# Optimization experiments

Hardware: AMD Instinct MI355X
Metric: run time of the kernel (lower is better)

The kernel has to match this reference:

```python
import jax, jax.numpy as jnp
import numpy as np

KH = KW = 3
STRIDE = 1
PAD = 1
DIL = 1


def _bilinear_sample(img, py, px):
    Hin, Win = img.shape[-2], img.shape[-1]
    y0 = jnp.floor(py)
    x0 = jnp.floor(px)
    y0i = y0.astype(jnp.int32)
    x0i = x0.astype(jnp.int32)
    wy = py - y0
    wx = px - x0

    def get(yi, xi):
        valid = (yi >= 0) & (yi < Hin) & (xi >= 0) & (xi < Win)
        yc = jnp.clip(yi, 0, Hin - 1)
        xc = jnp.clip(xi, 0, Win - 1)
        v = img[:, yc, xc]  # [C, K, H, W]
        return v * valid[None].astype(img.dtype)

    v00 = get(y0i, x0i)
    v01 = get(y0i, x0i + 1)
    v10 = get(y0i + 1, x0i)
    v11 = get(y0i + 1, x0i + 1)
    return (v00 * (1 - wy) * (1 - wx) + v01 * (1 - wy) * wx
            + v10 * wy * (1 - wx) + v11 * wy * wx)  # [C, K, H, W]


def _deform_conv(input, offset, mask, weight, bias):
    B, C, H, W = input.shape
    outH = (H + 2 * PAD - DIL * (KH - 1) - 1) // STRIDE + 1
    outW = (W + 2 * PAD - DIL * (KW - 1) - 1) // STRIDE + 1
    K = KH * KW
    # NOTE: DepthOffset in the original source overwrites its computed
    # depth-guided offsets with zeros and detaches them, so the effective
    # sampling offset is just `offset` (standard modulated deform conv, DCNv2).
    off = offset.reshape(B, K, 2, outH, outW)
    off_y = off[:, :, 0]  # [B, K, outH, outW]
    off_x = off[:, :, 1]
    ky = (jnp.arange(K) // KW) * DIL  # kernel-tap row offsets
    kx = (jnp.arange(K) % KW) * DIL
    ys = jnp.arange(outH) * STRIDE - PAD
    xs = jnp.arange(outW) * STRIDE - PAD
    base_y = (ky[:, None, None] + ys[None, :, None]).astype(input.dtype)  # [K, outH, 1]
    base_x = (kx[:, None, None] + xs[None, None, :]).astype(input.dtype)  # [K, 1, outW]
    py = base_y[None] + off_y  # [B, K, outH, outW]
    px = base_x[None] + off_x
    cols = jax.vmap(_bilinear_sample)(input, py, px)  # [B, C, K, outH, outW]
    cols = cols * mask[:, None]  # modulate by mask [B, 1, K, outH, outW]
    out = jnp.einsum('bckhw,ock->bohw', cols, weight.reshape(weight.shape[0], C, K))
    return out + bias[None, :, None, None]


def setup_inputs() -> dict:
    key = jax.random.key(0)
    ks = jax.random.split(key, 6)
    B, C, H, W = 4, 64, 128, 128
    O = 64
    fan_in = C * KH * KW
    bound = 1.0 / np.sqrt(fan_in)
    return {
        'input': jax.random.normal(ks[0], (B, C, H, W), dtype=jnp.float32),
        'depth': jax.random.uniform(ks[1], (B, 1, H, W), dtype=jnp.float32),
        'offset': jax.random.normal(ks[2], (B, 18, H, W), dtype=jnp.float32),
        'mask': jax.random.uniform(ks[3], (B, 9, H, W), dtype=jnp.float32),
        'weight': jax.random.uniform(ks[4], (O, C, KH, KW), dtype=jnp.float32,
                                     minval=-bound, maxval=bound),
        'bias': jax.random.uniform(ks[5], (O,), dtype=jnp.float32,
                                   minval=-bound, maxval=bound),
    }


def reference(input, depth, offset, mask, weight, bias):
    # depth-guided offsets are computed then zeroed+detached in the original
    # module, so depth does not influence the output.
    return _deform_conv(input, offset, mask, weight, bias)
```

## Files before the change

### kernel.cpp

```cpp
#include <hip/hip_runtime.h>


typedef __attribute__((ext_vector_type(8))) short bf16x8;
typedef __attribute__((ext_vector_type(4))) float f32x4;
typedef __attribute__((ext_vector_type(2))) float f32x2;
typedef __attribute__((ext_vector_type(4))) unsigned int u32x4;

#define HH 128
#define WW 128
#define CC 64
#define OO 64
#define HW (128 * 128)

__device__ __forceinline__ unsigned f32_to_bf16_rne(float f) {
    unsigned u = __float_as_uint(f);
    return (u + 0x7FFFu + ((u >> 16) & 1u)) >> 16;
}

__device__ __forceinline__ unsigned cvtpk_bf16(float lo, float hi) {
    unsigned r;
    asm("v_cvt_pk_bf16_f32 %0, %1, %2" : "=v"(r) : "v"(lo), "v"(hi));
    return r;
}

__global__ __launch_bounds__(256)
void prep_fused18(const float* __restrict__ input,
                  unsigned short* __restrict__ nhwc,
                  const float* __restrict__ weight,
                  unsigned short* __restrict__ wT2)
{
    __shared__ unsigned tile[64][33];
    const int tid = threadIdx.x;
    const int blk = blockIdx.x;

    if (blk >= 2048) {
        const int d  = (blk - 2048) * 256 + tid;
        const int o  = d & 63;
        const int k8 = d >> 6;
        const int kt = k8 >> 3;
        const int c8 = k8 & 7;
        u32x4 pk;
        #pragma unroll
        for (int jj = 0; jj < 4; ++jj) {
            unsigned lo = f32_to_bf16_rne(weight[o * 576 + (c8 * 8 + 2 * jj)     * 9 + kt]);
            unsigned hi = f32_to_bf16_rne(weight[o * 576 + (c8 * 8 + 2 * jj + 1) * 9 + kt]);
            pk[jj] = lo | (hi << 16);
        }
        *(u32x4*)(wT2 + (size_t)d * 8) = pk;
        return;
    }

    const int b  = blk >> 9;
    const int y  = (blk >> 2) & 127;
    const int xbase = (blk & 3) * 32;
    #pragma unroll
    for (int it = 0; it < 2; ++it) {
        int flat = it * 256 + tid;
        int c = flat >> 3, x4 = flat & 7;
        const f32x4 v = *(const f32x4*)(input + ((b * 64 + c) * 128 + y) * 128 + xbase + x4 * 4);
        tile[c][x4 * 4 + 0] = f32_to_bf16_rne(v[0]);
        tile[c][x4 * 4 + 1] = f32_to_bf16_rne(v[1]);
        tile[c][x4 * 4 + 2] = f32_to_bf16_rne(v[2]);
        tile[c][x4 * 4 + 3] = f32_to_bf16_rne(v[3]);
    }
    __syncthreads();
    {
        int x = tid >> 3, cg = tid & 7;
        unsigned r0 = tile[cg * 8 + 0][x], r1 = tile[cg * 8 + 1][x];
        unsigned r2 = tile[cg * 8 + 2][x], r3 = tile[cg * 8 + 3][x];
        unsigned r4 = tile[cg * 8 + 4][x], r5 = tile[cg * 8 + 5][x];
        unsigned r6 = tile[cg * 8 + 6][x], r7 = tile[cg * 8 + 7][x];
        u32x4 pk;
        pk[0] = r0 | (r1 << 16); pk[1] = r2 | (r3 << 16);
        pk[2] = r4 | (r5 << 16); pk[3] = r6 | (r7 << 16);
        *(u32x4*)(nhwc + ((size_t)((b * 128 + y) * 128 + xbase + x)) * 64 + cg * 8) = pk;
    }
}

__global__ __launch_bounds__(1024)
void ddc_order18(const unsigned short* __restrict__ nhwc,
                 const unsigned short* __restrict__ wT2,
                 const float* __restrict__ offset,
                 const float* __restrict__ mask,
                 const float* __restrict__ bias,
                 float* __restrict__ out)
{
    __shared__ u32x4 win[8192];
    __shared__ float sten[6912];

    const int blk0 = blockIdx.x;
    const int blk  = (blk0 & 7) * 32 + (blk0 >> 3);
    const int b    = blk >> 6;
    const int h0   = (blk & 63) * 2;
    const int ys   = h0 - 3;
    const int tid  = threadIdx.x;
    const int wave = tid >> 6;
    const int lane = tid & 63;
    const int l15  = lane & 15;
    const int kq   = lane >> 4;
    const int hr   = wave >> 3;
    const int h    = h0 + hr;
    const int wpix = (wave & 7) * 16 + l15;

    f32x4 acc[4];
    #pragma unroll
    for (int mt = 0; mt < 4; ++mt) acc[mt] = (f32x4){0.f, 0.f, 0.f, 0.f};

    const unsigned short* nb = nhwc + (size_t)b * HW * CC;
    const u32x4* wsrc = (const u32x4*)wT2;

    #pragma unroll
    for (int it = 0; it < 7; ++it) {
        const int f = it * 1024 + tid;
        if (f < 6912) {
            const int plane = f >> 8;
            const int fr    = (f >> 7) & 1;
            const int x     = f & 127;
            sten[f] = (plane < 18)
                ? offset[((b * 18 + plane)      * 128 + (h0 + fr)) * 128 + x]
                : mask  [((b * 9 + (plane - 18))* 128 + (h0 + fr)) * 128 + x];
        }
    }

    #pragma unroll
    for (int slot = 0; slot < 8; ++slot) {
        const int y = ys + slot;
        if (y >= 0 && y < HH) {
            const int q  = tid;
            const int x  = q >> 3;
            const int c8 = q & 7;
            win[slot * 1024 + q] =
                *(const u32x4*)(nb + ((size_t)(y * WW + x)) * CC + ((c8 ^ (x & 7)) << 3));
        }
    }
    __syncthreads();

    #pragma unroll
    for (int kt = 0; kt < 9; ++kt) {
        const u32x4* wpa = wsrc + (kt * 8 + kq)     * 64 + l15;
        const u32x4* wpb = wsrc + (kt * 8 + 4 + kq) * 64 + l15;
        const u32x4 wa0 = wpa[0], wa1 = wpa[16], wa2 = wpa[32], wa3 = wpa[48];
        const u32x4 wb0 = wpb[0], wb1 = wpb[16], wb2 = wpb[32], wb3 = wpb[48];

        const float oy = sten[(2 * kt)     * 256 + hr * 128 + wpix];
        const float ox = sten[(2 * kt + 1) * 256 + hr * 128 + wpix];
        const float m  = sten[(18 + kt)    * 256 + hr * 128 + wpix];

        const float py = (float)(h - 1 + kt / 3) + oy;
        const float px = (float)(wpix - 1 + kt % 3) + ox;
        const float y0f = floorf(py), x0f = floorf(px);
        const int y0 = (int)y0f, x0 = (int)x0f;
        const float wy = py - y0f, wx = px - x0f;
        const int y1 = y0 + 1, x1 = x0 + 1;
        const bool vy0 = (y0 >= 0) & (y0 < HH);
        const bool vy1 = (y1 >= 0) & (y1 < HH);
        const bool vx0 = (x0 >= 0) & (x0 < WW);
        const bool vx1 = (x1 >= 0) & (x1 < WW);
        const int y0c = min(max(y0, 0), HH - 1), y1c = min(max(y1, 0), HH - 1);
        const int x0c = min(max(x0, 0), WW - 1), x1c = min(max(x1, 0), WW - 1);
        const float wy1 = 1.f - wy, wx1 = 1.f - wx;
        const float c00 = (vy0 && vx0) ? wy1 * wx1 * m : 0.f;
        const float c01 = (vy0 && vx1) ? wy1 * wx  * m : 0.f;
        const float c10 = (vy1 && vx0) ? wy  * wx1 * m : 0.f;
        const float c11 = (vy1 && vx1) ? wy  * wx  * m : 0.f;

        const int s0 = y0c - ys, s1 = y1c - ys;
        const bool in0 = ((unsigned)s0 < 8u);
        const bool in1 = ((unsigned)s1 < 8u);
        const int bx0 = x0c * 8, sx0 = x0c & 7;
        const int bx1 = x1c * 8, sx1 = x1c & 7;

        u32x4 w00a, w01a, w00b, w01b;
        if (!in0) {
            const unsigned short* p0 = nb + ((size_t)y0c * WW + x0c) * CC;
            const unsigned short* p1 = nb + ((size_t)y0c * WW + x1c) * CC;
            w00a = *(const u32x4*)(p0 + kq * 8);
            w01a = *(const u32x4*)(p1 + kq * 8);
            w00b = *(const u32x4*)(p0 + 32 + kq * 8);
            w01b = *(const u32x4*)(p1 + 32 + kq * 8);
        } else {
            const int r0 = s0 * 1024;
            w00a = win[r0 + bx0 + (kq ^ sx0)];
            w01a = win[r0 + bx1 + (kq ^ sx1)];
            w00b = win[r0 + bx0 + ((4 + kq) ^ sx0)];
            w01b = win[r0 + bx1 + ((4 + kq) ^ sx1)];
        }
        u32x4 w10a, w11a, w10b, w11b;
        if (!in1) {
            const unsigned short* p0 = nb + ((size_t)y1c * WW + x0c) * CC;
            const unsigned short* p1 = nb + ((size_t)y1c * WW + x1c) * CC;
            w10a = *(const u32x4*)(p0 + kq * 8);
            w11a = *(const u32x4*)(p1 + kq * 8);
            w10b = *(const u32x4*)(p0 + 32 + kq * 8);
            w11b = *(const u32x4*)(p1 + 32 + kq * 8);
        } else {
            const int r1 = s1 * 1024;
            w10a = win[r1 + bx0 + (kq ^ sx0)];
            w11a = win[r1 + bx1 + (kq ^ sx1)];
            w10b = win[r1 + bx0 + ((4 + kq) ^ sx0)];
            w11b = win[r1 + bx1 + ((4 + kq) ^ sx1)];
        }

        const f32x2 vc00 = (f32x2){c00, c00}, vc01 = (f32x2){c01, c01};
        const f32x2 vc10 = (f32x2){c10, c10}, vc11 = (f32x2){c11, c11};

        #pragma unroll
        for (int ks = 0; ks < 2; ++ks) {
            const u32x4 w00 = ks ? w00b : w00a;
            const u32x4 w01 = ks ? w01b : w01a;
            const u32x4 w10 = ks ? w10b : w10a;
            const u32x4 w11 = ks ? w11b : w11a;
            u32x4 pk;
            #pragma unroll
            for (int j = 0; j < 4; ++j) {
                const f32x2 A = (f32x2){__uint_as_float(w00[j] << 16),
                                        __uint_as_float(w00[j] & 0xFFFF0000u)};
                const f32x2 B = (f32x2){__uint_as_float(w01[j] << 16),
                                        __uint_as_float(w01[j] & 0xFFFF0000u)};
                const f32x2 D = (f32x2){__uint_as_float(w10[j] << 16),
                                        __uint_as_float(w10[j] & 0xFFFF0000u)};
                const f32x2 E = (f32x2){__uint_as_float(w11[j] << 16),
                                        __uint_as_float(w11[j] & 0xFFFF0000u)};
                const f32x2 S = vc00 * A + vc01 * B + vc10 * D + vc11 * E;
                pk[j] = cvtpk_bf16(S[0], S[1]);
            }
            const bf16x8 bfrag = __builtin_bit_cast(bf16x8, pk);

            __builtin_amdgcn_s_setprio(1);
            acc[0] = __builtin_amdgcn_mfma_f32_16x16x32_bf16(
                __builtin_bit_cast(bf16x8, ks ? wb0 : wa0), bfrag, acc[0], 0, 0, 0);
            acc[1] = __builtin_amdgcn_mfma_f32_16x16x32_bf16(
                __builtin_bit_cast(bf16x8, ks ? wb1 : wa1), bfrag, acc[1], 0, 0, 0);
            acc[2] = __builtin_amdgcn_mfma_f32_16x16x32_bf16(
                __builtin_bit_cast(bf16x8, ks ? wb2 : wa2), bfrag, acc[2], 0, 0, 0);
            acc[3] = __builtin_amdgcn_mfma_f32_16x16x32_bf16(
                __builtin_bit_cast(bf16x8, ks ? wb3 : wa3), bfrag, acc[3], 0, 0, 0);
            __builtin_amdgcn_s_setprio(0);
        }
    }

    #pragma unroll
    for (int mt = 0; mt < 4; ++mt) {
        const f32x4 bv = *(const f32x4*)(bias + mt * 16 + kq * 4);
        #pragma unroll
        for (int r = 0; r < 4; ++r) {
            const int o = mt * 16 + kq * 4 + r;
            out[((b * 64 + o) * 128 + h) * 128 + wpix] = acc[mt][r] + bv[r];
        }
    }
}

extern "C" void kernel_launch(void* const* d_in, const int* in_sizes, int n_in,
                              void* d_out, int out_size, void* d_ws, size_t ws_size,
                              hipStream_t stream)
{
    const float* input  = (const float*)d_in[0];
    const float* offset = (const float*)d_in[2];
    const float* mask   = (const float*)d_in[3];
    const float* weight = (const float*)d_in[4];
    const float* bias   = (const float*)d_in[5];
    float* out = (float*)d_out;

    unsigned short* nhwc = (unsigned short*)d_ws;
    unsigned short* wT2  = nhwc + (size_t)4 * HW * CC;

    prep_fused18<<<dim3(2066), dim3(256), 0, stream>>>(input, nhwc, weight, wT2);
    ddc_order18<<<dim3(256), dim3(1024), 0, stream>>>(nhwc, wT2, offset, mask, bias, out);
}
```

Before: 108.0 us.

## Software-pipeline tap gathers with one-row blocks and register-held offsets

Each block now covers one output row with 512 threads (512 blocks, two blocks per CU) instead of two rows with 1024 threads. Offsets and mask are loaded straight into registers, so the shared stencil buffer is gone. The 9-tap loop is software-pipelined: the gathers and weight loads for tap k+1 are issued before the interpolation and MFMA of tap k, with sched_barriers to keep that order and the setprio calls removed. Each block still loads an 8-row shared window but now uses it for only one row, so window loads per output roughly double, and the double-buffered fragments raise register pressure.

```diff
diff --git a/kernel.cpp b/kernel.cpp
--- a/kernel.cpp
+++ b/kernel.cpp
@@ -24,7 +24,7 @@
 }
 
 __global__ __launch_bounds__(256)
-void prep_fused18(const float* __restrict__ input,
+void prep_fused19(const float* __restrict__ input,
                   unsigned short* __restrict__ nhwc,
                   const float* __restrict__ weight,
                   unsigned short* __restrict__ wT2)
@@ -77,30 +77,27 @@
     }
 }
 
-__global__ __launch_bounds__(1024)
-void ddc_order18(const unsigned short* __restrict__ nhwc,
-                 const unsigned short* __restrict__ wT2,
-                 const float* __restrict__ offset,
-                 const float* __restrict__ mask,
-                 const float* __restrict__ bias,
-                 float* __restrict__ out)
+__global__ __launch_bounds__(512, 2)
+void ddc_pipe19(const unsigned short* __restrict__ nhwc,
+                const unsigned short* __restrict__ wT2,
+                const float* __restrict__ offset,
+                const float* __restrict__ mask,
+                const float* __restrict__ bias,
+                float* __restrict__ out)
 {
     __shared__ u32x4 win[8192];
-    __shared__ float sten[6912];
 
     const int blk0 = blockIdx.x;
-    const int blk  = (blk0 & 7) * 32 + (blk0 >> 3);
-    const int b    = blk >> 6;
-    const int h0   = (blk & 63) * 2;
-    const int ys   = h0 - 3;
+    const int blk  = (blk0 & 7) * 64 + (blk0 >> 3);
+    const int b    = blk >> 7;
+    const int h    = blk & 127;
+    const int ys   = h - 3;
     const int tid  = threadIdx.x;
     const int wave = tid >> 6;
     const int lane = tid & 63;
     const int l15  = lane & 15;
     const int kq   = lane >> 4;
-    const int hr   = wave >> 3;
-    const int h    = h0 + hr;
-    const int wpix = (wave & 7) * 16 + l15;
+    const int wpix = wave * 16 + l15;
 
     f32x4 acc[4];
     #pragma unroll
@@ -109,24 +106,20 @@
     const unsigned short* nb = nhwc + (size_t)b * HW * CC;
     const u32x4* wsrc = (const u32x4*)wT2;
 
-    #pragma unroll
-    for (int it = 0; it < 7; ++it) {
-        const int f = it * 1024 + tid;
-        if (f < 6912) {
-            const int plane = f >> 8;
-            const int fr    = (f >> 7) & 1;
-            const int x     = f & 127;
-            sten[f] = (plane < 18)
-                ? offset[((b * 18 + plane)      * 128 + (h0 + fr)) * 128 + x]
-                : mask  [((b * 9 + (plane - 18))* 128 + (h0 + fr)) * 128 + x];
-        }
-    }
-
-    #pragma unroll
-    for (int slot = 0; slot < 8; ++slot) {
+    float oyv[9], oxv[9], mv[9];
+    #pragma unroll
+    for (int kt = 0; kt < 9; ++kt) {
+        oyv[kt] = offset[((b * 18 + 2 * kt)     * 128 + h) * 128 + wpix];
+        oxv[kt] = offset[((b * 18 + 2 * kt + 1) * 128 + h) * 128 + wpix];
+        mv[kt]  = mask  [((b * 9  + kt)         * 128 + h) * 128 + wpix];
+    }
+
+    #pragma unroll
+    for (int i = 0; i < 16; ++i) {
+        const int slot = i >> 1;
         const int y = ys + slot;
         if (y >= 0 && y < HH) {
-            const int q  = tid;
+            const int q  = ((i & 1) << 9) + tid;
             const int x  = q >> 3;
             const int c8 = q & 7;
             win[slot * 1024 + q] =
@@ -135,17 +128,12 @@
     }
     __syncthreads();
 
-    #pragma unroll
-    for (int kt = 0; kt < 9; ++kt) {
-        const u32x4* wpa = wsrc + (kt * 8 + kq)     * 64 + l15;
-        const u32x4* wpb = wsrc + (kt * 8 + 4 + kq) * 64 + l15;
-        const u32x4 wa0 = wpa[0], wa1 = wpa[16], wa2 = wpa[32], wa3 = wpa[48];
-        const u32x4 wb0 = wpb[0], wb1 = wpb[16], wb2 = wpb[32], wb3 = wpb[48];
-
-        const float oy = sten[(2 * kt)     * 256 + hr * 128 + wpix];
-        const float ox = sten[(2 * kt + 1) * 256 + hr * 128 + wpix];
-        const float m  = sten[(18 + kt)    * 256 + hr * 128 + wpix];
-
+    u32x4 cb[2][8];
+    u32x4 wb[2][8];
+    float pc[2][4];
+
+    auto prepare = [&](int kt, int sl) {
+        const float oy = oyv[kt], ox = oxv[kt], m = mv[kt];
         const float py = (float)(h - 1 + kt / 3) + oy;
         const float px = (float)(wpix - 1 + kt % 3) + ox;
         const float y0f = floorf(py), x0f = floorf(px);
@@ -159,10 +147,10 @@
         const int y0c = min(max(y0, 0), HH - 1), y1c = min(max(y1, 0), HH - 1);
         const int x0c = min(max(x0, 0), WW - 1), x1c = min(max(x1, 0), WW - 1);
         const float wy1 = 1.f - wy, wx1 = 1.f - wx;
-        const float c00 = (vy0 && vx0) ? wy1 * wx1 * m : 0.f;
-        const float c01 = (vy0 && vx1) ? wy1 * wx  * m : 0.f;
-        const float c10 = (vy1 && vx0) ? wy  * wx1 * m : 0.f;
-        const float c11 = (vy1 && vx1) ? wy  * wx  * m : 0.f;
+        pc[sl][0] = (vy0 && vx0) ? wy1 * wx1 * m : 0.f;
+        pc[sl][1] = (vy0 && vx1) ? wy1 * wx  * m : 0.f;
+        pc[sl][2] = (vy1 && vx0) ? wy  * wx1 * m : 0.f;
+        pc[sl][3] = (vy1 && vx1) ? wy  * wx  * m : 0.f;
 
         const int s0 = y0c - ys, s1 = y1c - ys;
         const bool in0 = ((unsigned)s0 < 8u);
@@ -170,46 +158,54 @@
         const int bx0 = x0c * 8, sx0 = x0c & 7;
         const int bx1 = x1c * 8, sx1 = x1c & 7;
 
-        u32x4 w00a, w01a, w00b, w01b;
+        const u32x4* wpa = wsrc + (kt * 8 + kq)     * 64 + l15;
+        const u32x4* wpb = wsrc + (kt * 8 + 4 + kq) * 64 + l15;
+        wb[sl][0] = wpa[0];  wb[sl][1] = wpa[16];
+        wb[sl][2] = wpa[32]; wb[sl][3] = wpa[48];
+        wb[sl][4] = wpb[0];  wb[sl][5] = wpb[16];
+        wb[sl][6] = wpb[32]; wb[sl][7] = wpb[48];
+
         if (!in0) {
             const unsigned short* p0 = nb + ((size_t)y0c * WW + x0c) * CC;
             const unsigned short* p1 = nb + ((size_t)y0c * WW + x1c) * CC;
-            w00a = *(const u32x4*)(p0 + kq * 8);
-            w01a = *(const u32x4*)(p1 + kq * 8);
-            w00b = *(const u32x4*)(p0 + 32 + kq * 8);
-            w01b = *(const u32x4*)(p1 + 32 + kq * 8);
+            cb[sl][0] = *(const u32x4*)(p0 + kq * 8);
+            cb[sl][1] = *(const u32x4*)(p1 + kq * 8);
+            cb[sl][4] = *(const u32x4*)(p0 + 32 + kq * 8);
+            cb[sl][5] = *(const u32x4*)(p1 + 32 + kq * 8);
         } else {
             const int r0 = s0 * 1024;
-            w00a = win[r0 + bx0 + (kq ^ sx0)];
-            w01a = win[r0 + bx1 + (kq ^ sx1)];
-            w00b = win[r0 + bx0 + ((4 + kq) ^ sx0)];
-            w01b = win[r0 + bx1 + ((4 + kq) ^ sx1)];
-        }
-        u32x4 w10a, w11a, w10b, w11b;
+            cb[sl][0] = win[r0 + bx0 + (kq ^ sx0)];
+            cb[sl][1] = win[r0 + bx1 + (kq ^ sx1)];
+            cb[sl][4] = win[r0 + bx0 + ((4 + kq) ^ sx0)];
+            cb[sl][5] = win[r0 + bx1 + ((4 + kq) ^ sx1)];
+        }
         if (!in1) {
             const unsigned short* p0 = nb + ((size_t)y1c * WW + x0c) * CC;
             const unsigned short* p1 = nb + ((size_t)y1c * WW + x1c) * CC;
-            w10a = *(const u32x4*)(p0 + kq * 8);
-            w11a = *(const u32x4*)(p1 + kq * 8);
-            w10b = *(const u32x4*)(p0 + 32 + kq * 8);
-            w11b = *(const u32x4*)(p1 + 32 + kq * 8);
+            cb[sl][2] = *(const u32x4*)(p0 + kq * 8);
+            cb[sl][3] = *(const u32x4*)(p1 + kq * 8);
+            cb[sl][6] = *(const u32x4*)(p0 + 32 + kq * 8);
+            cb[sl][7] = *(const u32x4*)(p1 + 32 + kq * 8);
         } else {
             const int r1 = s1 * 1024;
-            w10a = win[r1 + bx0 + (kq ^ sx0)];
-            w11a = win[r1 + bx1 + (kq ^ sx1)];
-            w10b = win[r1 + bx0 + ((4 + kq) ^ sx0)];
-            w11b = win[r1 + bx1 + ((4 + kq) ^ sx1)];
-        }
-
-        const f32x2 vc00 = (f32x2){c00, c00}, vc01 = (f32x2){c01, c01};
-        const f32x2 vc10 = (f32x2){c10, c10}, vc11 = (f32x2){c11, c11};
-
+            cb[sl][2] = win[r1 + bx0 + (kq ^ sx0)];
+            cb[sl][3] = win[r1 + bx1 + (kq ^ sx1)];
+            cb[sl][6] = win[r1 + bx0 + ((4 + kq) ^ sx0)];
+            cb[sl][7] = win[r1 + bx1 + ((4 + kq) ^ sx1)];
+        }
+    };
+
+    auto consume = [&](int sl) {
+        const f32x2 vc00 = (f32x2){pc[sl][0], pc[sl][0]};
+        const f32x2 vc01 = (f32x2){pc[sl][1], pc[sl][1]};
+        const f32x2 vc10 = (f32x2){pc[sl][2], pc[sl][2]};
+        const f32x2 vc11 = (f32x2){pc[sl][3], pc[sl][3]};
         #pragma unroll
         for (int ks = 0; ks < 2; ++ks) {
-            const u32x4 w00 = ks ? w00b : w00a;
-            const u32x4 w01 = ks ? w01b : w01a;
-            const u32x4 w10 = ks ? w10b : w10a;
-            const u32x4 w11 = ks ? w11b : w11a;
+            const u32x4 w00 = cb[sl][ks * 4 + 0];
+            const u32x4 w01 = cb[sl][ks * 4 + 1];
+            const u32x4 w10 = cb[sl][ks * 4 + 2];
+            const u32x4 w11 = cb[sl][ks * 4 + 3];
             u32x4 pk;
             #pragma unroll
             for (int j = 0; j < 4; ++j) {
@@ -225,18 +221,24 @@
                 pk[j] = cvtpk_bf16(S[0], S[1]);
             }
             const bf16x8 bfrag = __builtin_bit_cast(bf16x8, pk);
-
-            __builtin_amdgcn_s_setprio(1);
             acc[0] = __builtin_amdgcn_mfma_f32_16x16x32_bf16(
-                __builtin_bit_cast(bf16x8, ks ? wb0 : wa0), bfrag, acc[0], 0, 0, 0);
+                __builtin_bit_cast(bf16x8, wb[sl][ks * 4 + 0]), bfrag, acc[0], 0, 0, 0);
             acc[1] = __builtin_amdgcn_mfma_f32_16x16x32_bf16(
-                __builtin_bit_cast(bf16x8, ks ? wb1 : wa1), bfrag, acc[1], 0, 0, 0);
+                __builtin_bit_cast(bf16x8, wb[sl][ks * 4 + 1]), bfrag, acc[1], 0, 0, 0);
             acc[2] = __builtin_amdgcn_mfma_f32_16x16x32_bf16(
-                __builtin_bit_cast(bf16x8, ks ? wb2 : wa2), bfrag, acc[2], 0, 0, 0);
+                __builtin_bit_cast(bf16x8, wb[sl][ks * 4 + 2]), bfrag, acc[2], 0, 0, 0);
             acc[3] = __builtin_amdgcn_mfma_f32_16x16x32_bf16(
-                __builtin_bit_cast(bf16x8, ks ? wb3 : wa3), bfrag, acc[3], 0, 0, 0);
-            __builtin_amdgcn_s_setprio(0);
-        }
+                __builtin_bit_cast(bf16x8, wb[sl][ks * 4 + 3]), bfrag, acc[3], 0, 0, 0);
+        }
+    };
+
+    prepare(0, 0);
+    #pragma unroll
+    for (int kt = 0; kt < 9; ++kt) {
+        if (kt < 8) prepare(kt + 1, (kt + 1) & 1);
+        __builtin_amdgcn_sched_barrier(0);
+        consume(kt & 1);
+        __builtin_amdgcn_sched_barrier(0);
     }
 
     #pragma unroll
@@ -264,6 +266,6 @@
     unsigned short* nhwc = (unsigned short*)d_ws;
     unsigned short* wT2  = nhwc + (size_t)4 * HW * CC;
 
-    prep_fused18<<<dim3(2066), dim3(256), 0, stream>>>(input, nhwc, weight, wT2);
-    ddc_order18<<<dim3(256), dim3(1024), 0, stream>>>(nhwc, wT2, offset, mask, bias, out);
-}
+    prep_fused19<<<dim3(2066), dim3(256), 0, stream>>>(input, nhwc, weight, wT2);
+    ddc_pipe19<<<dim3(512), dim3(512), 0, stream>>>(nhwc, wT2, offset, mask, bias, out);
+}
```

Result: no change. 106.5 us (-1.4%).
